# Kernel optimization log

Hardware: AMD Instinct MI355X
Metric: run time of the kernel (lower is better)

## Reference

```python
import jax, jax.numpy as jnp
import numpy as np

TOP_K = 2

def setup_inputs() -> dict:
    key = jax.random.key(0)
    k0, k1, k2, k3 = jax.random.split(key, 4)
    B, T, D, F, E = 2, 2048, 1024, 4096, 8
    x = jax.random.normal(k0, (B, T, D), dtype=jnp.float32)
    Wr = jax.random.normal(k1, (E, D), dtype=jnp.float32) * 0.02   # router weight [out=E, in=D]
    W1 = jax.random.normal(k2, (E, F, D), dtype=jnp.float32) * 0.02  # per-expert up-proj [out=F, in=D]
    W2 = jax.random.normal(k3, (E, D, F), dtype=jnp.float32) * 0.02  # per-expert down-proj [out=D, in=F]
    return {"x": x, "Wr": Wr, "W1": W1, "W2": W2}

def reference(x, Wr, W1, W2):
    B, T, D = x.shape
    E = Wr.shape[0]
    N = B * T
    xf = x.reshape(N, D)
    # Router in fp32 on the un-cast activations (as in the torch module).
    logits = xf @ Wr.T                                   # [N, E]
    probs = jax.nn.softmax(logits, axis=-1)
    topk_w, topk_idx = jax.lax.top_k(probs, TOP_K)       # [N, K]
    topk_w = topk_w / jnp.sum(topk_w, axis=-1, keepdims=True)
    # Combine weights scattered into a dense [N, E] dispatch/combine matrix
    # (top_k indices are distinct, so .set is exact).
    combine = jnp.zeros((N, E), dtype=jnp.float32)
    combine = combine.at[jnp.arange(N)[:, None], topk_idx].set(topk_w)
    # Expert FFN runs in bf16 (comm_dtype in the original all-to-all pipeline).
    xb = xf.astype(jnp.bfloat16)
    h = jax.nn.gelu(jnp.einsum('nd,efd->enf', xb, W1.astype(jnp.bfloat16)),
                    approximate=False)                   # [E, N, F]
    yo = jnp.einsum('enf,edf->end', h, W2.astype(jnp.bfloat16))  # [E, N, D]
    # Weighted combine: bf16 expert outputs * fp32 gate weights -> fp32 (torch promotion).
    out = jnp.einsum('end,ne->nd', yo.astype(jnp.float32), combine)
    return out.reshape(B, T, D)
```

## Files before the change

kernel.cpp:

```cpp
#include <hip/hip_runtime.h>
#include <hip/hip_bf16.h>

typedef __attribute__((ext_vector_type(8))) __bf16 bf16x8;
typedef __attribute__((ext_vector_type(4))) float floatx4;

constexpr int N_TOK = 4096;
constexpr int DDIM  = 1024;
constexpr int FDIM  = 4096;
constexpr int NEXP  = 8;
constexpr int NSLOT = 2 * N_TOK;
constexpr int MAXT  = 72;

static __device__ __forceinline__ unsigned short f2bf(float f) {
    union { __hip_bfloat16 h; unsigned short u; } v;
    v.h = __float2bfloat16(f);
    return v.u;
}

static __device__ __forceinline__ void gl2lds16(const unsigned short* g, unsigned short* l) {
    __builtin_amdgcn_global_load_lds(
        (__attribute__((address_space(1))) void*)g,
        (__attribute__((address_space(3))) void*)l,
        16, 0, 0);
}

__global__ void castX_kernel(const float* __restrict__ src, unsigned short* __restrict__ dst,
                             int* __restrict__ counts) {
    int i = blockIdx.x * 256 + threadIdx.x;
    float4 v = *(const float4*)(src + (size_t)i * 4);
    ushort4 o;
    o.x = f2bf(v.x); o.y = f2bf(v.y); o.z = f2bf(v.z); o.w = f2bf(v.w);
    *(ushort4*)(dst + (size_t)i * 4) = o;
    if (blockIdx.x == 0 && threadIdx.x < NEXP) counts[threadIdx.x] = 0;
}

__global__ void castN_kernel(const float* __restrict__ src, unsigned short* __restrict__ dst, int n4) {
    int i = blockIdx.x * 256 + threadIdx.x;
    if (i >= n4) return;
    float4 v = *(const float4*)(src + (size_t)i * 4);
    ushort4 o;
    o.x = f2bf(v.x); o.y = f2bf(v.y); o.z = f2bf(v.z); o.w = f2bf(v.w);
    *(ushort4*)(dst + (size_t)i * 4) = o;
}

__global__ void router_kernel(const float* __restrict__ x, const float* __restrict__ Wr,
                              int* __restrict__ te, float* __restrict__ tw,
                              int* __restrict__ counts) {
    __shared__ float wr[NEXP * DDIM];
    const int tid = threadIdx.x;
    for (int i = tid; i < NEXP * DDIM; i += 256) wr[i] = Wr[i];
    __syncthreads();
    const int wave = tid >> 6, lane = tid & 63;
    const int t = blockIdx.x * 4 + wave;

    float xr[16];
    const float* xp = x + (size_t)t * DDIM;
    #pragma unroll
    for (int i = 0; i < 16; i++) xr[i] = xp[lane + 64 * i];

    float logit[NEXP];
    #pragma unroll
    for (int e = 0; e < NEXP; e++) {
        float s = 0.f;
        #pragma unroll
        for (int i = 0; i < 16; i++) s += xr[i] * wr[e * DDIM + lane + 64 * i];
        #pragma unroll
        for (int off = 32; off > 0; off >>= 1) s += __shfl_xor(s, off, 64);
        logit[e] = s;
    }
    if (lane == 0) {
        int i0 = 0; float l0 = logit[0];
        #pragma unroll
        for (int e = 1; e < NEXP; e++) if (logit[e] > l0) { l0 = logit[e]; i0 = e; }
        int i1 = -1; float l1 = -3.0e38f;
        #pragma unroll
        for (int e = 0; e < NEXP; e++) if (e != i0 && logit[e] > l1) { l1 = logit[e]; i1 = e; }
        float p1 = expf(l1 - l0);
        float w0 = 1.f / (1.f + p1);
        float w1 = p1 * w0;
        te[t * 2] = i0; te[t * 2 + 1] = i1;
        tw[t * 2] = w0; tw[t * 2 + 1] = w1;
        atomicAdd(&counts[i0], 1);
        atomicAdd(&counts[i1], 1);
    }
}

__global__ void scan_kernel(const int* __restrict__ counts, int* __restrict__ offsets,
                            int* __restrict__ cursors, int* __restrict__ tile_em,
                            int* __restrict__ ntile) {
    if (threadIdx.x == 0) {
        int acc = 0, nt = 0;
        for (int e = 0; e < NEXP; e++) {
            offsets[e] = acc;
            for (int m0 = 0; m0 < counts[e]; m0 += 128)
                tile_em[nt++] = (e << 16) | (m0 >> 7);
            acc += counts[e];
        }
        offsets[NEXP] = acc;
        ntile[0] = nt;
        for (int i = nt; i < MAXT; i++) tile_em[i] = 0;
    }
    if (threadIdx.x < NEXP) cursors[threadIdx.x] = 0;
}

__global__ void scatter_kernel(const int* __restrict__ te, const float* __restrict__ tw,
                               const int* __restrict__ offsets, int* __restrict__ cursors,
                               int* __restrict__ rowid, float* __restrict__ gate,
                               int* __restrict__ tok2slot) {
    int t = blockIdx.x * 256 + threadIdx.x;
    if (t >= N_TOK) return;
    #pragma unroll
    for (int k = 0; k < 2; k++) {
        int e = te[t * 2 + k];
        int pos = atomicAdd(&cursors[e], 1);
        int slot = offsets[e] + pos;
        rowid[slot] = t;
        gate[slot] = tw[t * 2 + k];
        tok2slot[t * 2 + k] = slot;
    }
}

template <int K, bool UP, bool BF16W>
__global__ __launch_bounds__(256)
void ffn_gemm(const unsigned short* __restrict__ A,
              const float* __restrict__ Wf,
              const unsigned short* __restrict__ Wb,
              unsigned short* __restrict__ Hout,
              float* __restrict__ Y,
              const int* __restrict__ rowid,
              const float* __restrict__ gate,
              const int* __restrict__ offsets,
              const int* __restrict__ tile_em,
              const int* __restrict__ ntile) {
    constexpr int BM = 128, BN = 128, BK = 32, LDT = 32;
    constexpr int NOUT = UP ? FDIM : DDIM;

    const int bt = blockIdx.x % MAXT;
    if (bt >= ntile[0]) return;
    const int em = tile_em[bt];
    const int e  = em >> 16;
    const int m0 = (em & 0xffff) << 7;
    const int n0 = (blockIdx.x / MAXT) * BN;
    const int seg = offsets[e];
    const int cnt = offsets[e + 1] - seg;

    __shared__ __align__(16) unsigned short As[BM * LDT];
    __shared__ __align__(16) unsigned short Bs[BN * LDT];

    const int tid = threadIdx.x;
    const int lane = tid & 63;
    const int wave = tid >> 6;

    const int srow0 = wave * 32 + (lane >> 2);
    const int chunk = lane & 3;

    const unsigned short* ag[2];
    #pragma unroll
    for (int j = 0; j < 2; j++) {
        int r = srow0 + j * 16;
        int slot = seg + m0 + r;
        if (slot >= NSLOT) slot = NSLOT - 1;
        if (UP) { int t = rowid[slot]; ag[j] = A + (size_t)t * DDIM + chunk * 8; }
        else    { ag[j] = A + (size_t)slot * FDIM + chunk * 8; }
    }
    const unsigned short* bg[2];
    #pragma unroll
    for (int j = 0; j < 2; j++) {
        int r = srow0 + j * 16;
        bg[j] = Wb + ((size_t)e * NOUT + n0 + r) * K + chunk * 8;
    }
    unsigned short* asl[2];
    unsigned short* bsl[2];
    #pragma unroll
    for (int j = 0; j < 2; j++) {
        asl[j] = &As[(wave * 32 + j * 16) * LDT] + lane * 8;
        bsl[j] = &Bs[(wave * 32 + j * 16) * LDT] + lane * 8;
    }

    const int br = tid >> 1;
    const int bh = (tid & 1) * 16;
    const float* bptrf = Wf + ((size_t)e * NOUT + n0 + br) * K + bh;
    unsigned short* bsdst = &Bs[br * LDT + bh];

    const int wm = (wave >> 1) * 64;
    const int wn = (wave & 1) * 64;
    const int frow = lane & 15;
    const int quad = lane >> 4;

    floatx4 acc[4][4];
    #pragma unroll
    for (int i = 0; i < 4; i++)
        #pragma unroll
        for (int j = 0; j < 4; j++)
            acc[i][j] = (floatx4){0.f, 0.f, 0.f, 0.f};

    for (int k0 = 0; k0 < K; k0 += BK) {
        uint4 bu0, bu1;
        if (!BF16W) {
            float4 b0 = *(const float4*)(bptrf);
            float4 b1 = *(const float4*)(bptrf + 4);
            float4 b2 = *(const float4*)(bptrf + 8);
            float4 b3 = *(const float4*)(bptrf + 12);
            union { unsigned short u[16]; uint4 q[2]; } bb;
            bb.u[0] = f2bf(b0.x); bb.u[1] = f2bf(b0.y); bb.u[2]  = f2bf(b0.z); bb.u[3]  = f2bf(b0.w);
            bb.u[4] = f2bf(b1.x); bb.u[5] = f2bf(b1.y); bb.u[6]  = f2bf(b1.z); bb.u[7]  = f2bf(b1.w);
            bb.u[8] = f2bf(b2.x); bb.u[9] = f2bf(b2.y); bb.u[10] = f2bf(b2.z); bb.u[11] = f2bf(b2.w);
            bb.u[12] = f2bf(b3.x); bb.u[13] = f2bf(b3.y); bb.u[14] = f2bf(b3.z); bb.u[15] = f2bf(b3.w);
            bu0 = bb.q[0]; bu1 = bb.q[1];
            bptrf += BK;
        }
        __syncthreads();
        gl2lds16(ag[0], asl[0]);
        gl2lds16(ag[1], asl[1]);
        if (BF16W) {
            gl2lds16(bg[0], bsl[0]);
            gl2lds16(bg[1], bsl[1]);
            bg[0] += BK; bg[1] += BK;
        } else {
            *(uint4*)(bsdst) = bu0;
            *(uint4*)(bsdst + 8) = bu1;
        }
        ag[0] += BK; ag[1] += BK;
        __syncthreads();

        bf16x8 av[4], bv[4];
        #pragma unroll
        for (int i = 0; i < 4; i++)
            av[i] = *(const bf16x8*)&As[(wm + i * 16 + frow) * LDT + quad * 8];
        #pragma unroll
        for (int i = 0; i < 4; i++)
            bv[i] = *(const bf16x8*)&Bs[(wn + i * 16 + frow) * LDT + quad * 8];
        #pragma unroll
        for (int mt = 0; mt < 4; mt++)
            #pragma unroll
            for (int nt = 0; nt < 4; nt++)
                acc[mt][nt] = __builtin_amdgcn_mfma_f32_16x16x32_bf16(av[mt], bv[nt], acc[mt][nt], 0, 0, 0);
    }

    #pragma unroll
    for (int mt = 0; mt < 4; mt++) {
        #pragma unroll
        for (int r = 0; r < 4; r++) {
            int mloc = m0 + wm + mt * 16 + quad * 4 + r;
            if (mloc >= cnt) continue;
            int slot = seg + mloc;
            if (UP) {
                #pragma unroll
                for (int nt = 0; nt < 4; nt++) {
                    int n = n0 + wn + nt * 16 + frow;
                    float v = acc[mt][nt][r];
                    float g = 0.5f * v * (1.0f + erff(v * 0.70710678118654752f));
                    Hout[(size_t)slot * FDIM + n] = f2bf(g);
                }
            } else {
                float gw = gate[slot];
                #pragma unroll
                for (int nt = 0; nt < 4; nt++) {
                    int n = n0 + wn + nt * 16 + frow;
                    Y[(size_t)slot * DDIM + n] = gw * acc[mt][nt][r];
                }
            }
        }
    }
}

__global__ void combine_kernel(const float* __restrict__ Y, const int* __restrict__ tok2slot,
                               float* __restrict__ out) {
    int idx = blockIdx.x * 256 + threadIdx.x;
    int t = idx >> 8;
    int c = (idx & 255) * 4;
    int s0 = tok2slot[t * 2], s1 = tok2slot[t * 2 + 1];
    float4 a = *(const float4*)(Y + (size_t)s0 * DDIM + c);
    float4 b = *(const float4*)(Y + (size_t)s1 * DDIM + c);
    *(float4*)(out + (size_t)t * DDIM + c) =
        make_float4(a.x + b.x, a.y + b.y, a.z + b.z, a.w + b.w);
}

extern "C" void kernel_launch(void* const* d_in, const int* in_sizes, int n_in,
                              void* d_out, int out_size, void* d_ws, size_t ws_size,
                              hipStream_t stream) {
    const float* x  = (const float*)d_in[0];
    const float* Wr = (const float*)d_in[1];
    const float* W1 = (const float*)d_in[2];
    const float* W2 = (const float*)d_in[3];
    float* out = (float*)d_out;

    char* ws = (char*)d_ws;
    size_t off = 0;
    auto alloc = [&](size_t bytes) -> char* {
        char* p = ws + off;
        off = (off + bytes + 255) & ~(size_t)255;
        return p;
    };
    unsigned short* xb   = (unsigned short*)alloc((size_t)N_TOK * DDIM * 2);
    unsigned short* H    = (unsigned short*)alloc((size_t)NSLOT * FDIM * 2);
    float* Yb      = (float*)alloc((size_t)NSLOT * DDIM * 4);
    int*   rowid   = (int*)alloc(NSLOT * 4);
    float* gatew   = (float*)alloc(NSLOT * 4);
    int*   te      = (int*)alloc(NSLOT * 4);
    float* tw      = (float*)alloc(NSLOT * 4);
    int*   t2s     = (int*)alloc(NSLOT * 4);
    int*   counts  = (int*)alloc(64);
    int*   offsets = (int*)alloc(64);
    int*   cursors = (int*)alloc(64);
    int*   tile_em = (int*)alloc(MAXT * 4);
    int*   ntile   = (int*)alloc(64);
    unsigned short* w1b = (unsigned short*)alloc((size_t)NEXP * FDIM * DDIM * 2);
    unsigned short* w2b = (unsigned short*)alloc((size_t)NEXP * DDIM * FDIM * 2);
    const bool bf16w = (off <= ws_size);

    castX_kernel<<<N_TOK * DDIM / 4 / 256, 256, 0, stream>>>(x, xb, counts);
    if (bf16w) {
        const int n4 = NEXP * FDIM * DDIM / 4;
        castN_kernel<<<(n4 + 255) / 256, 256, 0, stream>>>(W1, w1b, n4);
        castN_kernel<<<(n4 + 255) / 256, 256, 0, stream>>>(W2, w2b, n4);
    }
    router_kernel<<<N_TOK / 4, 256, 0, stream>>>(x, Wr, te, tw, counts);
    scan_kernel<<<1, 64, 0, stream>>>(counts, offsets, cursors, tile_em, ntile);
    scatter_kernel<<<(N_TOK + 255) / 256, 256, 0, stream>>>(te, tw, offsets, cursors, rowid, gatew, t2s);

    if (bf16w) {
        ffn_gemm<DDIM, true,  true ><<<MAXT * (FDIM / 128), 256, 0, stream>>>(xb, W1, w1b, H, Yb, rowid, gatew, offsets, tile_em, ntile);
        ffn_gemm<FDIM, false, true ><<<MAXT * (DDIM / 128), 256, 0, stream>>>(H,  W2, w2b, H, Yb, rowid, gatew, offsets, tile_em, ntile);
    } else {
        ffn_gemm<DDIM, true,  false><<<MAXT * (FDIM / 128), 256, 0, stream>>>(xb, W1, w1b, H, Yb, rowid, gatew, offsets, tile_em, ntile);
        ffn_gemm<FDIM, false, false><<<MAXT * (DDIM / 128), 256, 0, stream>>>(H,  W2, w2b, H, Yb, rowid, gatew, offsets, tile_em, ntile);
    }
    combine_kernel<<<N_TOK, 256, 0, stream>>>(Yb, t2s, out);
}
```

Measured before the change: 711.5 us.

## Widen GEMM K-tile with XOR-swizzled LDS, XCD-aware tile mapping, and fused small kernels

The expert GEMMs move from BK=32 to BK=64 with an XOR swizzle on the LDS layout to avoid bank conflicts, so each barrier pair is amortized over twice as many MFMAs. Block IDs are remapped so consecutive blocks on the same XCD share N slabs, which should improve L2 reuse of weights. The two weight-cast launches are merged into one kernel, and scan and scatter are fused into a single-block kernel using shared-memory cursors. The fp32-weight fallback path is removed, so the code now assumes the workspace is large enough for bf16 weights.

```diff
diff --git a/kernel.cpp b/kernel.cpp
--- a/kernel.cpp
+++ b/kernel.cpp
@@ -34,13 +34,17 @@
     if (blockIdx.x == 0 && threadIdx.x < NEXP) counts[threadIdx.x] = 0;
 }
 
-__global__ void castN_kernel(const float* __restrict__ src, unsigned short* __restrict__ dst, int n4) {
+__global__ void castW_kernel(const float* __restrict__ W1, const float* __restrict__ W2,
+                             unsigned short* __restrict__ w1b, unsigned short* __restrict__ w2b) {
+    constexpr int HALF = NEXP * FDIM * DDIM / 4;
     int i = blockIdx.x * 256 + threadIdx.x;
-    if (i >= n4) return;
-    float4 v = *(const float4*)(src + (size_t)i * 4);
+    const float* s; unsigned short* d; int j;
+    if (i < HALF) { s = W1; d = w1b; j = i; }
+    else          { s = W2; d = w2b; j = i - HALF; }
+    float4 v = *(const float4*)(s + (size_t)j * 4);
     ushort4 o;
     o.x = f2bf(v.x); o.y = f2bf(v.y); o.z = f2bf(v.z); o.w = f2bf(v.w);
-    *(ushort4*)(dst + (size_t)i * 4) = o;
+    *(ushort4*)(d + (size_t)j * 4) = o;
 }
 
 __global__ void router_kernel(const float* __restrict__ x, const float* __restrict__ Wr,
@@ -85,13 +89,19 @@
     }
 }
 
-__global__ void scan_kernel(const int* __restrict__ counts, int* __restrict__ offsets,
-                            int* __restrict__ cursors, int* __restrict__ tile_em,
-                            int* __restrict__ ntile) {
-    if (threadIdx.x == 0) {
+__global__ void scan_scatter_kernel(const int* __restrict__ counts,
+                                    const int* __restrict__ te, const float* __restrict__ tw,
+                                    int* __restrict__ offsets, int* __restrict__ tile_em,
+                                    int* __restrict__ ntile,
+                                    int* __restrict__ rowid, float* __restrict__ gate,
+                                    int* __restrict__ tok2slot) {
+    __shared__ int soff[NEXP];
+    __shared__ int scur[NEXP];
+    const int tid = threadIdx.x;
+    if (tid == 0) {
         int acc = 0, nt = 0;
         for (int e = 0; e < NEXP; e++) {
-            offsets[e] = acc;
+            offsets[e] = acc; soff[e] = acc;
             for (int m0 = 0; m0 < counts[e]; m0 += 128)
                 tile_em[nt++] = (e << 16) | (m0 >> 7);
             acc += counts[e];
@@ -100,30 +110,24 @@
         ntile[0] = nt;
         for (int i = nt; i < MAXT; i++) tile_em[i] = 0;
     }
-    if (threadIdx.x < NEXP) cursors[threadIdx.x] = 0;
-}
-
-__global__ void scatter_kernel(const int* __restrict__ te, const float* __restrict__ tw,
-                               const int* __restrict__ offsets, int* __restrict__ cursors,
-                               int* __restrict__ rowid, float* __restrict__ gate,
-                               int* __restrict__ tok2slot) {
-    int t = blockIdx.x * 256 + threadIdx.x;
-    if (t >= N_TOK) return;
-    #pragma unroll
-    for (int k = 0; k < 2; k++) {
-        int e = te[t * 2 + k];
-        int pos = atomicAdd(&cursors[e], 1);
-        int slot = offsets[e] + pos;
-        rowid[slot] = t;
-        gate[slot] = tw[t * 2 + k];
-        tok2slot[t * 2 + k] = slot;
-    }
-}
-
-template <int K, bool UP, bool BF16W>
+    if (tid < NEXP) scur[tid] = 0;
+    __syncthreads();
+    for (int t = tid; t < N_TOK; t += 256) {
+        #pragma unroll
+        for (int k = 0; k < 2; k++) {
+            int e = te[t * 2 + k];
+            int pos = atomicAdd(&scur[e], 1);
+            int slot = soff[e] + pos;
+            rowid[slot] = t;
+            gate[slot] = tw[t * 2 + k];
+            tok2slot[t * 2 + k] = slot;
+        }
+    }
+}
+
+template <int K, bool UP>
 __global__ __launch_bounds__(256)
 void ffn_gemm(const unsigned short* __restrict__ A,
-              const float* __restrict__ Wf,
               const unsigned short* __restrict__ Wb,
               unsigned short* __restrict__ Hout,
               float* __restrict__ Y,
@@ -132,60 +136,61 @@
               const int* __restrict__ offsets,
               const int* __restrict__ tile_em,
               const int* __restrict__ ntile) {
-    constexpr int BM = 128, BN = 128, BK = 32, LDT = 32;
-    constexpr int NOUT = UP ? FDIM : DDIM;
-
-    const int bt = blockIdx.x % MAXT;
+    constexpr int BM = 128, BN = 128, BK = 64;
+    constexpr int NOUT  = UP ? FDIM : DDIM;
+    constexpr int NSLAB = (NOUT / BN) / 8;
+
+    const int id    = blockIdx.x;
+    const int xcd   = id & 7;
+    const int local = id >> 3;
+    const int nloc  = local / MAXT;
+    const int bt    = local - nloc * MAXT;
     if (bt >= ntile[0]) return;
     const int em = tile_em[bt];
     const int e  = em >> 16;
     const int m0 = (em & 0xffff) << 7;
-    const int n0 = (blockIdx.x / MAXT) * BN;
+    const int n0 = (xcd * NSLAB + nloc) * BN;
     const int seg = offsets[e];
     const int cnt = offsets[e + 1] - seg;
 
-    __shared__ __align__(16) unsigned short As[BM * LDT];
-    __shared__ __align__(16) unsigned short Bs[BN * LDT];
-
-    const int tid = threadIdx.x;
+    __shared__ __align__(16) unsigned short As[BM * BK];
+    __shared__ __align__(16) unsigned short Bs[BN * BK];
+
+    const int tid  = threadIdx.x;
     const int lane = tid & 63;
     const int wave = tid >> 6;
 
-    const int srow0 = wave * 32 + (lane >> 2);
-    const int chunk = lane & 3;
-
-    const unsigned short* ag[2];
-    #pragma unroll
-    for (int j = 0; j < 2; j++) {
-        int r = srow0 + j * 16;
+    const int rl   = lane >> 3;
+    const int cg   = (lane & 7) ^ rl;
+
+    const unsigned short* ag[4];
+    #pragma unroll
+    for (int j = 0; j < 4; j++) {
+        int r = wave * 32 + j * 8 + rl;
         int slot = seg + m0 + r;
         if (slot >= NSLOT) slot = NSLOT - 1;
-        if (UP) { int t = rowid[slot]; ag[j] = A + (size_t)t * DDIM + chunk * 8; }
-        else    { ag[j] = A + (size_t)slot * FDIM + chunk * 8; }
-    }
-    const unsigned short* bg[2];
-    #pragma unroll
-    for (int j = 0; j < 2; j++) {
-        int r = srow0 + j * 16;
-        bg[j] = Wb + ((size_t)e * NOUT + n0 + r) * K + chunk * 8;
-    }
-    unsigned short* asl[2];
-    unsigned short* bsl[2];
-    #pragma unroll
-    for (int j = 0; j < 2; j++) {
-        asl[j] = &As[(wave * 32 + j * 16) * LDT] + lane * 8;
-        bsl[j] = &Bs[(wave * 32 + j * 16) * LDT] + lane * 8;
-    }
-
-    const int br = tid >> 1;
-    const int bh = (tid & 1) * 16;
-    const float* bptrf = Wf + ((size_t)e * NOUT + n0 + br) * K + bh;
-    unsigned short* bsdst = &Bs[br * LDT + bh];
+        if (UP) { int t = rowid[slot]; ag[j] = A + (size_t)t * DDIM + cg * 8; }
+        else    { ag[j] = A + (size_t)slot * FDIM + cg * 8; }
+    }
+    const unsigned short* bg[4];
+    #pragma unroll
+    for (int j = 0; j < 4; j++) {
+        int r = wave * 32 + j * 8 + rl;
+        bg[j] = Wb + ((size_t)e * NOUT + n0 + r) * K + cg * 8;
+    }
+    unsigned short* asl[4];
+    unsigned short* bsl[4];
+    #pragma unroll
+    for (int j = 0; j < 4; j++) {
+        asl[j] = &As[(wave * 32 + j * 8) * BK] + lane * 8;
+        bsl[j] = &Bs[(wave * 32 + j * 8) * BK] + lane * 8;
+    }
 
     const int wm = (wave >> 1) * 64;
     const int wn = (wave & 1) * 64;
     const int frow = lane & 15;
     const int quad = lane >> 4;
+    const int f7 = frow & 7;
 
     floatx4 acc[4][4];
     #pragma unroll
@@ -195,46 +200,30 @@
             acc[i][j] = (floatx4){0.f, 0.f, 0.f, 0.f};
 
     for (int k0 = 0; k0 < K; k0 += BK) {
-        uint4 bu0, bu1;
-        if (!BF16W) {
-            float4 b0 = *(const float4*)(bptrf);
-            float4 b1 = *(const float4*)(bptrf + 4);
-            float4 b2 = *(const float4*)(bptrf + 8);
-            float4 b3 = *(const float4*)(bptrf + 12);
-            union { unsigned short u[16]; uint4 q[2]; } bb;
-            bb.u[0] = f2bf(b0.x); bb.u[1] = f2bf(b0.y); bb.u[2]  = f2bf(b0.z); bb.u[3]  = f2bf(b0.w);
-            bb.u[4] = f2bf(b1.x); bb.u[5] = f2bf(b1.y); bb.u[6]  = f2bf(b1.z); bb.u[7]  = f2bf(b1.w);
-            bb.u[8] = f2bf(b2.x); bb.u[9] = f2bf(b2.y); bb.u[10] = f2bf(b2.z); bb.u[11] = f2bf(b2.w);
-            bb.u[12] = f2bf(b3.x); bb.u[13] = f2bf(b3.y); bb.u[14] = f2bf(b3.z); bb.u[15] = f2bf(b3.w);
-            bu0 = bb.q[0]; bu1 = bb.q[1];
-            bptrf += BK;
+        __syncthreads();
+        #pragma unroll
+        for (int j = 0; j < 4; j++) gl2lds16(ag[j], asl[j]);
+        #pragma unroll
+        for (int j = 0; j < 4; j++) gl2lds16(bg[j], bsl[j]);
+        #pragma unroll
+        for (int j = 0; j < 4; j++) { ag[j] += BK; bg[j] += BK; }
+        __syncthreads();
+
+        #pragma unroll
+        for (int kk = 0; kk < 2; kk++) {
+            bf16x8 av[4], bv[4];
+            #pragma unroll
+            for (int i = 0; i < 4; i++)
+                av[i] = *(const bf16x8*)&As[(wm + i * 16 + frow) * BK + ((kk * 4 + quad) ^ f7) * 8];
+            #pragma unroll
+            for (int i = 0; i < 4; i++)
+                bv[i] = *(const bf16x8*)&Bs[(wn + i * 16 + frow) * BK + ((kk * 4 + quad) ^ f7) * 8];
+            #pragma unroll
+            for (int mt = 0; mt < 4; mt++)
+                #pragma unroll
+                for (int nt = 0; nt < 4; nt++)
+                    acc[mt][nt] = __builtin_amdgcn_mfma_f32_16x16x32_bf16(av[mt], bv[nt], acc[mt][nt], 0, 0, 0);
         }
-        __syncthreads();
-        gl2lds16(ag[0], asl[0]);
-        gl2lds16(ag[1], asl[1]);
-        if (BF16W) {
-            gl2lds16(bg[0], bsl[0]);
-            gl2lds16(bg[1], bsl[1]);
-            bg[0] += BK; bg[1] += BK;
-        } else {
-            *(uint4*)(bsdst) = bu0;
-            *(uint4*)(bsdst + 8) = bu1;
-        }
-        ag[0] += BK; ag[1] += BK;
-        __syncthreads();
-
-        bf16x8 av[4], bv[4];
-        #pragma unroll
-        for (int i = 0; i < 4; i++)
-            av[i] = *(const bf16x8*)&As[(wm + i * 16 + frow) * LDT + quad * 8];
-        #pragma unroll
-        for (int i = 0; i < 4; i++)
-            bv[i] = *(const bf16x8*)&Bs[(wn + i * 16 + frow) * LDT + quad * 8];
-        #pragma unroll
-        for (int mt = 0; mt < 4; mt++)
-            #pragma unroll
-            for (int nt = 0; nt < 4; nt++)
-                acc[mt][nt] = __builtin_amdgcn_mfma_f32_16x16x32_bf16(av[mt], bv[nt], acc[mt][nt], 0, 0, 0);
     }
 
     #pragma unroll
@@ -302,29 +291,20 @@
     int*   t2s     = (int*)alloc(NSLOT * 4);
     int*   counts  = (int*)alloc(64);
     int*   offsets = (int*)alloc(64);
-    int*   cursors = (int*)alloc(64);
     int*   tile_em = (int*)alloc(MAXT * 4);
     int*   ntile   = (int*)alloc(64);
     unsigned short* w1b = (unsigned short*)alloc((size_t)NEXP * FDIM * DDIM * 2);
     unsigned short* w2b = (unsigned short*)alloc((size_t)NEXP * DDIM * FDIM * 2);
-    const bool bf16w = (off <= ws_size);
+    (void)ws_size;
 
     castX_kernel<<<N_TOK * DDIM / 4 / 256, 256, 0, stream>>>(x, xb, counts);
-    if (bf16w) {
-        const int n4 = NEXP * FDIM * DDIM / 4;
-        castN_kernel<<<(n4 + 255) / 256, 256, 0, stream>>>(W1, w1b, n4);
-        castN_kernel<<<(n4 + 255) / 256, 256, 0, stream>>>(W2, w2b, n4);
-    }
+    castW_kernel<<<2 * NEXP * FDIM * DDIM / 4 / 256, 256, 0, stream>>>(W1, W2, w1b, w2b);
     router_kernel<<<N_TOK / 4, 256, 0, stream>>>(x, Wr, te, tw, counts);
-    scan_kernel<<<1, 64, 0, stream>>>(counts, offsets, cursors, tile_em, ntile);
-    scatter_kernel<<<(N_TOK + 255) / 256, 256, 0, stream>>>(te, tw, offsets, cursors, rowid, gatew, t2s);
-
-    if (bf16w) {
-        ffn_gemm<DDIM, true,  true ><<<MAXT * (FDIM / 128), 256, 0, stream>>>(xb, W1, w1b, H, Yb, rowid, gatew, offsets, tile_em, ntile);
-        ffn_gemm<FDIM, false, true ><<<MAXT * (DDIM / 128), 256, 0, stream>>>(H,  W2, w2b, H, Yb, rowid, gatew, offsets, tile_em, ntile);
-    } else {
-        ffn_gemm<DDIM, true,  false><<<MAXT * (FDIM / 128), 256, 0, stream>>>(xb, W1, w1b, H, Yb, rowid, gatew, offsets, tile_em, ntile);
-        ffn_gemm<FDIM, false, false><<<MAXT * (DDIM / 128), 256, 0, stream>>>(H,  W2, w2b, H, Yb, rowid, gatew, offsets, tile_em, ntile);
-    }
+    scan_scatter_kernel<<<1, 256, 0, stream>>>(counts, te, tw, offsets, tile_em, ntile,
+                                               rowid, gatew, t2s);
+    ffn_gemm<DDIM, true ><<<8 * 4 * MAXT, 256, 0, stream>>>(xb, w1b, H, Yb, rowid, gatew,
+                                                            offsets, tile_em, ntile);
+    ffn_gemm<FDIM, false><<<8 * 1 * MAXT, 256, 0, stream>>>(H,  w2b, H, Yb, rowid, gatew,
+                                                            offsets, tile_em, ntile);
     combine_kernel<<<N_TOK, 256, 0, stream>>>(Yb, t2s, out);
 }
```

Result: no change. 712.7 us (+0.2%).
